# Optimization experiments

Measured on AMD Instinct MI355X. Metric: run time of the kernel, lower is better.

## Reference

```python
import jax, jax.numpy as jnp
import numpy as np

HIDDEN = 1024
NUM_HEADS = 16
HEAD_DIM = HIDDEN // NUM_HEADS
EPS = 1e-12


def _layernorm(x, g, b):
    mu = jnp.mean(x, axis=-1, keepdims=True)
    var = jnp.var(x, axis=-1, keepdims=True)
    return (x - mu) * jax.lax.rsqrt(var + EPS) * g + b


def _attention(q, k, v, mask, Wd, bd, ln_g, ln_b):
    # q: [B,T,H], k/v: [B,S,H], mask: [B,1,1,S] additive
    B, T, _ = q.shape
    S = k.shape[1]
    qh = q.reshape(B, T, NUM_HEADS, HEAD_DIM).transpose(0, 2, 1, 3)  # [B,h,T,d]
    kh = k.reshape(B, S, NUM_HEADS, HEAD_DIM).transpose(0, 2, 1, 3)
    vh = v.reshape(B, S, NUM_HEADS, HEAD_DIM).transpose(0, 2, 1, 3)
    scores = jnp.einsum('bhtd,bhsd->bhts', qh, kh) / jnp.sqrt(jnp.float32(HEAD_DIM))
    if mask is not None:
        scores = scores + mask
    probs = jax.nn.softmax(scores, axis=-1)  # dropout = identity in eval
    ctx = jnp.einsum('bhts,bhsd->bthd', probs, vh)  # [B,T,h,d]
    # torch: w = dense.weight.t().view(h, d, H); einsum('bfnd,ndh->bfh')
    w = Wd.T.reshape(NUM_HEADS, HEAD_DIM, HIDDEN)
    proj = jnp.einsum('bthd,hdH->btH', ctx, w) + bd
    # residual is the (projected) query tensor q, per source
    return _layernorm(q + proj, ln_g, ln_b)


def setup_inputs() -> dict:
    key = jax.random.key(0)
    ks = jax.random.split(key, 12)
    s = 0.02
    B, S, T = 4, 1024, 1024
    return {
        'encoder_states': jax.random.normal(ks[0], (B, S, HIDDEN), jnp.float32),
        'decoder_inputs': jax.random.normal(ks[1], (B, T, HIDDEN), jnp.float32),
        'src_attention_mask': jnp.zeros((B, 1, 1, S), jnp.float32),
        'tgt_attention_mask': jnp.zeros((B, 1, 1, T), jnp.float32),
        'Wq': jax.random.normal(ks[2], (HIDDEN, HIDDEN), jnp.float32) * s,
        'bq': jnp.zeros((HIDDEN,), jnp.float32),
        'Wk': jax.random.normal(ks[3], (HIDDEN, HIDDEN), jnp.float32) * s,
        'bk': jnp.zeros((HIDDEN,), jnp.float32),
        'Wv': jax.random.normal(ks[4], (HIDDEN, HIDDEN), jnp.float32) * s,
        'bv': jnp.zeros((HIDDEN,), jnp.float32),
        'Wd': jax.random.normal(ks[5], (HIDDEN, HIDDEN), jnp.float32) * s,
        'bd': jnp.zeros((HIDDEN,), jnp.float32),
        'ln_g': jnp.ones((HIDDEN,), jnp.float32),
        'ln_b': jnp.zeros((HIDDEN,), jnp.float32),
    }


def reference(encoder_states, decoder_inputs, src_attention_mask, tgt_attention_mask,
              Wq, bq, Wk, bk, Wv, bv, Wd, bd, ln_g, ln_b):
    # projections (torch Linear: x @ W.T + b)
    q1 = decoder_inputs @ Wq.T + bq
    k1 = decoder_inputs @ Wk.T + bk
    v1 = decoder_inputs @ Wv.T + bv
    ek = encoder_states @ Wk.T + bk
    ev = encoder_states @ Wv.T + bv
    # self-attention over decoder states
    self_out = _attention(q1, k1, v1, tgt_attention_mask, Wd, bd, ln_g, ln_b)
    # cross-attention: query = self_out directly (no extra projection, per source)
    out = _attention(self_out, ek, ev, src_attention_mask, Wd, bd, ln_g, ln_b)
    return out
```

## Files before the change

### kernel.cpp

```cpp
#include <hip/hip_runtime.h>
#include <stdint.h>


#define B_   4
#define T_   1024
#define S_   1024
#define H_   1024
#define LOG2E 1.44269504088896340736f
#define SCALE_K (0.125f * LOG2E)

typedef __attribute__((ext_vector_type(8)))  __bf16       bf16x8;
typedef __attribute__((ext_vector_type(4)))  float        f32x4;
typedef __attribute__((ext_vector_type(16))) float        f32x16;
typedef __attribute__((ext_vector_type(4)))  unsigned int uint4v;

static __device__ __forceinline__ float bf2f(unsigned int u) {
    return __builtin_bit_cast(float, u << 16);
}
static __device__ __forceinline__ unsigned short f2bf(float f) {
    unsigned int x = __builtin_bit_cast(unsigned int, f);
    return (unsigned short)((x + 0x7fffu + ((x >> 16) & 1u)) >> 16);
}
static __device__ __forceinline__ unsigned int cvt_pk_bf16(float lo, float hi) {
    unsigned int r;
    asm("v_cvt_pk_bf16_f32 %0, %1, %2" : "=v"(r) : "v"(lo), "v"(hi));
    return r;
}
static __device__ __forceinline__ void perm32swap(unsigned int& a, unsigned int& b) {
    asm("v_permlane32_swap_b32 %0, %1" : "+v"(a), "+v"(b));
}
static __device__ __forceinline__ f32x4 mfma16(bf16x8 a, bf16x8 b, f32x4 c) {
    return __builtin_amdgcn_mfma_f32_16x16x32_bf16(a, b, c, 0, 0, 0);
}
static __device__ __forceinline__ f32x16 mfma32(bf16x8 a, bf16x8 b, f32x16 c) {
    return __builtin_amdgcn_mfma_f32_32x32x16_bf16(a, b, c, 0, 0, 0);
}

typedef const __attribute__((address_space(1))) void gv_t;
typedef __attribute__((address_space(3))) void lv_t;
static __device__ __forceinline__ void g2lds16(const void* g, void* l) {
    __builtin_amdgcn_global_load_lds((gv_t*)(size_t)g, (lv_t*)(unsigned int)(size_t)l, 16, 0, 0);
}

struct CvtArgs {
    const float* src[6];
    unsigned short* dst[6];
    float scale[6];
    int n4[6];
};
__global__ __launch_bounds__(256)
void cvt_multi(CvtArgs a) {
    const int k = blockIdx.y;
    const int i = blockIdx.x * 256 + threadIdx.x;
    if (i >= a.n4[k]) return;
    const float s = a.scale[k];
    float4 v = ((const float4*)a.src[k])[i];
    uint2 o;
    o.x = (unsigned)f2bf(v.x * s) | ((unsigned)f2bf(v.y * s) << 16);
    o.y = (unsigned)f2bf(v.z * s) | ((unsigned)f2bf(v.w * s) << 16);
    ((uint2*)a.dst[k])[i] = o;
}

struct GemmJob {
    const unsigned short* A[5];
    const unsigned short* W[5];
    const float* bias[5];
    float bs[5];
    unsigned short* O[5];
    unsigned short* OT[5];
};
__global__ __launch_bounds__(256, 2)
void gemm_bf16(GemmJob job)
{
    __shared__ char smem[32768];
    char* As = smem;
    char* Bs = smem + 16384;
    const int tid = threadIdx.x;
    const int lane = tid & 63;
    const int w = tid >> 6;
    const int c = lane & 15, g = lane >> 4;
    const int wm = (w >> 1) * 64, wn = (w & 1) * 64;
    const int m0 = blockIdx.x * 128;
    const int set = blockIdx.y >> 3;
    const int n0 = (blockIdx.y & 7) * 128;
    const unsigned short* A    = job.A[set];
    const unsigned short* W    = job.W[set];
    const float* bias          = job.bias[set];
    const float bscale         = job.bs[set];
    unsigned short* O          = job.O[set];
    unsigned short* OT         = job.OT[set];

    f32x4 acc[4][4];
#pragma unroll
    for (int i = 0; i < 4; i++)
#pragma unroll
        for (int j = 0; j < 4; j++) acc[i][j] = (f32x4){0.f, 0.f, 0.f, 0.f};

    const int srow = w * 32 + (lane >> 3);
    const int swzc = ((lane & 7) ^ (lane >> 3)) * 8;
    const unsigned short* gA = A + (size_t)(m0 + srow) * 1024 + swzc;
    const unsigned short* gB = W + (size_t)(n0 + srow) * 1024 + swzc;
    char* lA = As + w * 4096;
    char* lB = Bs + w * 4096;

    for (int kk = 0; kk < 1024; kk += 64) {
#pragma unroll
        for (int q = 0; q < 4; q++) {
            g2lds16(gA + kk + q*8192, lA + q*1024);
            g2lds16(gB + kk + q*8192, lB + q*1024);
        }
        __syncthreads();
#pragma unroll
        for (int ksub = 0; ksub < 2; ksub++) {
            bf16x8 af[4], bfr[4];
#pragma unroll
            for (int t = 0; t < 4; t++) {
                const int ra = wm + t*16 + c;
                const int rb = wn + t*16 + c;
                const int so = ((ksub*4 + g) ^ (c & 7)) << 4;
                af[t]  = *(const bf16x8*)(As + ra*128 + so);
                bfr[t] = *(const bf16x8*)(Bs + rb*128 + so);
            }
#pragma unroll
            for (int i = 0; i < 4; i++)
#pragma unroll
                for (int j = 0; j < 4; j++)
                    acc[i][j] = mfma16(af[i], bfr[j], acc[i][j]);
        }
        __syncthreads();
    }

    float bvv[4];
#pragma unroll
    for (int j = 0; j < 4; j++) bvv[j] = bias[n0 + wn + j*16 + c] * bscale;

    if (OT == nullptr) {
        char* eb = As + w * 4096;
#pragma unroll
        for (int p = 0; p < 2; p++) {
#pragma unroll
            for (int ii = 0; ii < 2; ii++) {
                const int i = p*2 + ii;
#pragma unroll
                for (int j = 0; j < 4; j++)
#pragma unroll
                    for (int r = 0; r < 4; r++)
                        *(unsigned short*)(eb + (ii*16 + g*4 + r)*128 + (c + j*16)*2)
                            = f2bf(acc[i][j][r] + bvv[j]);
            }
            asm volatile("s_waitcnt lgkmcnt(0)" ::: "memory");
#pragma unroll
            for (int it = 0; it < 4; it++) {
                const int lrow = it*8 + (lane >> 3);
                uint4 vv = *(const uint4*)(eb + lrow*128 + (lane & 7)*16);
                *(uint4*)(O + (size_t)(m0 + wm + p*32 + lrow)*1024 + n0 + wn + (lane & 7)*8) = vv;
            }
            if (p == 0) asm volatile("s_waitcnt lgkmcnt(0)" ::: "memory");
        }
    } else {
        char* ebT = smem + w * 8192;
        const int n_glob = n0 + wn + lane;
        const int hh = n_glob >> 6, dd = n_glob & 63;
        const int bidx = m0 >> 10;
        unsigned short* vout0 = OT + ((size_t)((bidx*16 + hh)*64 + dd))*S_ + (m0 & 1023) + wm;
#pragma unroll
        for (int p = 0; p < 2; p++) {
#pragma unroll
            for (int ii = 0; ii < 2; ii++) {
                const int i = p*2 + ii;
#pragma unroll
                for (int j = 0; j < 4; j++) {
                    uint2 pw;
                    pw.x = (unsigned)f2bf(acc[i][j][0] + bvv[j]) |
                           ((unsigned)f2bf(acc[i][j][1] + bvv[j]) << 16);
                    pw.y = (unsigned)f2bf(acc[i][j][2] + bvv[j]) |
                           ((unsigned)f2bf(acc[i][j][3] + bvv[j]) << 16);
                    *(uint2*)(ebT + (j*16 + c)*72 + (ii*16 + g*4)*2) = pw;
                }
            }
            asm volatile("s_waitcnt lgkmcnt(0)" ::: "memory");
            unsigned short* vout = vout0 + p*32;
#pragma unroll
            for (int q = 0; q < 4; q++) {
                uint2 r0 = *(const uint2*)(ebT + lane*72 + (q*2    )*8);
                uint2 r1 = *(const uint2*)(ebT + lane*72 + (q*2 + 1)*8);
                uint4 vv; vv.x = r0.x; vv.y = r0.y; vv.z = r1.x; vv.w = r1.y;
                *(uint4*)(vout + q*8) = vv;
            }
            if (p == 0) asm volatile("s_waitcnt lgkmcnt(0)" ::: "memory");
        }
    }
}

__global__ __launch_bounds__(256, 4)
void attn_fused2(const unsigned short* __restrict__ Q,
                 const unsigned short* __restrict__ Kx,
                 const unsigned short* __restrict__ VT,
                 const float* __restrict__ mask,
                 unsigned short* __restrict__ Octx)
{
    __shared__ char smem[32768 + 4096 + 512 + 16];
    float* mb   = (float*)(smem + 32768);
    float* lbuf = (float*)(smem + 32768 + 4096);
    int* flag   = (int*)(smem + 32768 + 4096 + 512);

    const int tid = threadIdx.x;
    const int lane = tid & 63, w = tid >> 6;
    const int qc = lane & 31, hi = lane >> 5;
    const int bh = blockIdx.x, b = bh >> 4, h = bh & 15;
    const int q0 = blockIdx.y * 128 + w * 32;

    const int r0 = tid >> 3, sg = tid & 7;
    const unsigned short* gK0 = Kx + (size_t)(b*S_ + r0)*H_  + h*64 + sg*8;
    const unsigned short* gK1 = gK0 + (size_t)32*H_;
    const unsigned short* gV0 = VT + (size_t)(bh*64 + r0)*S_ + sg*8;
    const unsigned short* gV1 = gV0 + (size_t)32*S_;
    const int woff = r0*128 + ((sg*16) ^ ((r0 & 7) << 4));

    const unsigned short* qptr = Q + (size_t)(b*T_ + q0 + qc)*H_ + h*64 + hi*8;
    bf16x8 qf[4];
#pragma unroll
    for (int s = 0; s < 4; s++) qf[s] = *(const bf16x8*)(qptr + s*16);

    uint4 cK0 = *(const uint4*)gK0;
    uint4 cK1 = *(const uint4*)gK1;
    uint4 cV0 = *(const uint4*)gV0;
    uint4 cV1 = *(const uint4*)gV1;

    if (tid == 0) *flag = 0;
    __syncthreads();
    {
        float4 mv = ((const float4*)(mask + (size_t)b*S_))[tid];
        float4 ms;
        ms.x = mv.x * LOG2E; ms.y = mv.y * LOG2E; ms.z = mv.z * LOG2E; ms.w = mv.w * LOG2E;
        ((float4*)mb)[tid] = ms;
        if (mv.x != 0.f || mv.y != 0.f || mv.z != 0.f || mv.w != 0.f) atomicOr(flag, 1);
    }
    {
        char* b0 = smem;
        *(uint4*)(b0 + woff)               = cK0;
        *(uint4*)(b0 + 4096 + woff)        = cK1;
        *(uint4*)(b0 + 8192 + woff)        = cV0;
        *(uint4*)(b0 + 8192 + 4096 + woff) = cV1;
    }
    __syncthreads();
    const int msk = *flag;

    f32x16 o0 = {}, o1 = {};
    float lacc = 0.f;

    for (int t = 0; t < 16; ++t) {
        uint4 nK0, nK1, nV0, nV1;
        if (t < 15) {
            const size_t ko = (size_t)(t + 1) * 64 * H_;
            const int    vo = (t + 1) * 64;
            nK0 = *(const uint4*)(gK0 + ko);
            nK1 = *(const uint4*)(gK1 + ko);
            nV0 = *(const uint4*)(gV0 + vo);
            nV1 = *(const uint4*)(gV1 + vo);
        }
        char* Ks = smem + (t & 1) * 16384;
        char* Vs = Ks + 8192;

#pragma unroll
        for (int ts = 0; ts < 2; ++ts) {
            f32x16 st = {};
            __builtin_amdgcn_s_setprio(1);
#pragma unroll
            for (int step = 0; step < 4; ++step) {
                bf16x8 ak = *(const bf16x8*)(Ks + (ts*32 + qc)*128 +
                             ((step*32 + hi*16) ^ ((qc & 7) << 4)));
                st = mfma32(ak, qf[step], st);
            }
            __builtin_amdgcn_s_setprio(0);

            float pv[16];
            if (msk) {
#pragma unroll
                for (int rq = 0; rq < 4; ++rq) {
                    const float4 bb = *(const float4*)(mb + t*64 + ts*32 + rq*8 + hi*4);
#pragma unroll
                    for (int e = 0; e < 4; ++e)
                        pv[rq*4 + e] = __builtin_amdgcn_exp2f(st[rq*4 + e] + (&bb.x)[e]);
                }
            } else {
#pragma unroll
                for (int r = 0; r < 16; ++r) pv[r] = __builtin_amdgcn_exp2f(st[r]);
            }
#pragma unroll
            for (int r = 0; r < 16; ++r) lacc += pv[r];

#pragma unroll
            for (int half = 0; half < 2; ++half) {
                unsigned w0 = cvt_pk_bf16(pv[half*8 + 0], pv[half*8 + 1]);
                unsigned w1 = cvt_pk_bf16(pv[half*8 + 2], pv[half*8 + 3]);
                unsigned w2 = cvt_pk_bf16(pv[half*8 + 4], pv[half*8 + 5]);
                unsigned w3 = cvt_pk_bf16(pv[half*8 + 6], pv[half*8 + 7]);
                perm32swap(w0, w2);
                perm32swap(w1, w3);
                uint4v fw; fw[0] = w0; fw[1] = w1; fw[2] = w2; fw[3] = w3;
                const bf16x8 pa = __builtin_bit_cast(bf16x8, fw);
                const int scol = (ts*64 + half*32 + hi*16) ^ ((qc & 7) << 4);
                bf16x8 v0 = *(const bf16x8*)(Vs + qc*128        + scol);
                bf16x8 v1 = *(const bf16x8*)(Vs + (32 + qc)*128 + scol);
                __builtin_amdgcn_s_setprio(1);
                o0 = mfma32(pa, v0, o0);
                o1 = mfma32(pa, v1, o1);
                __builtin_amdgcn_s_setprio(0);
            }
        }

        if (t < 15) {
            char* nxt = smem + ((t + 1) & 1) * 16384;
            *(uint4*)(nxt + woff)               = nK0;
            *(uint4*)(nxt + 4096 + woff)        = nK1;
            *(uint4*)(nxt + 8192 + woff)        = nV0;
            *(uint4*)(nxt + 8192 + 4096 + woff) = nV1;
        }
        __syncthreads();
    }

    {
        unsigned la = __builtin_bit_cast(unsigned, lacc);
        unsigned lb = la;
        perm32swap(la, lb);
        const float ltot = __builtin_bit_cast(float, la) + __builtin_bit_cast(float, lb);
        const float linv = 1.f / ltot;
        if (hi == 0) lbuf[w*32 + qc] = linv;
    }
    __syncthreads();
    float4 li[4];
#pragma unroll
    for (int rq = 0; rq < 4; ++rq)
        li[rq] = *(const float4*)(lbuf + w*32 + rq*8 + hi*4);

#pragma unroll
    for (int dt = 0; dt < 2; ++dt) {
        const f32x16& oo = dt ? o1 : o0;
#pragma unroll
        for (int r = 0; r < 16; ++r) {
            const int qrow = (r & 3) + 8*(r >> 2) + 4*hi;
            const float val = oo[r] * (&li[r >> 2].x)[r & 3];
            Octx[(size_t)(b*T_ + q0 + qrow)*H_ + h*64 + dt*32 + qc] = f2bf(val);
        }
    }
}

template<int OUTMODE>
__global__ __launch_bounds__(256)
void ln_kernel(const unsigned short* __restrict__ resid,
               const unsigned short* __restrict__ proj,
               const float* __restrict__ gam,
               const float* __restrict__ bet,
               unsigned short* __restrict__ obf,
               float* __restrict__ of32)
{
    __shared__ float red[8];
    const int tid = threadIdx.x;
    const int lane = tid & 63, w = tid >> 6;
    const int i = tid * 4;
    const size_t base = (size_t)blockIdx.x * 1024 + i;
    uint2 rv = *(const uint2*)(resid + base);
    uint2 pv = *(const uint2*)(proj + base);
    float x[4];
    x[0] = bf2f(rv.x & 0xffffu) + bf2f(pv.x & 0xffffu);
    x[1] = bf2f(rv.x >> 16)     + bf2f(pv.x >> 16);
    x[2] = bf2f(rv.y & 0xffffu) + bf2f(pv.y & 0xffffu);
    x[3] = bf2f(rv.y >> 16)     + bf2f(pv.y >> 16);
    float s = x[0] + x[1] + x[2] + x[3];
    float q = x[0]*x[0] + x[1]*x[1] + x[2]*x[2] + x[3]*x[3];
#pragma unroll
    for (int off = 1; off < 64; off <<= 1) {
        s += __shfl_xor(s, off);
        q += __shfl_xor(q, off);
    }
    if (lane == 0) { red[w*2] = s; red[w*2 + 1] = q; }
    __syncthreads();
    s = red[0] + red[2] + red[4] + red[6];
    q = red[1] + red[3] + red[5] + red[7];
    const float mu   = s * (1.f/1024.f);
    const float var  = q * (1.f/1024.f) - mu*mu;
    const float rstd = rsqrtf(var + 1e-12f);
    const float4 gv = *(const float4*)(gam + i);
    const float4 bv = *(const float4*)(bet + i);
    float y[4];
#pragma unroll
    for (int j = 0; j < 4; j++)
        y[j] = (x[j] - mu) * rstd * (&gv.x)[j] + (&bv.x)[j];
    if (OUTMODE == 0) {
        uint2 oo;
        oo.x = (unsigned)f2bf(y[0]) | ((unsigned)f2bf(y[1]) << 16);
        oo.y = (unsigned)f2bf(y[2]) | ((unsigned)f2bf(y[3]) << 16);
        *(uint2*)(obf + base) = oo;
    } else {
        float4 oo; oo.x = y[0]; oo.y = y[1]; oo.z = y[2]; oo.w = y[3];
        *(float4*)(of32 + base) = oo;
    }
}

extern "C" void kernel_launch(void* const* d_in, const int* in_sizes, int n_in,
                              void* d_out, int out_size, void* d_ws, size_t ws_size,
                              hipStream_t stream)
{
    const float* enc   = (const float*)d_in[0];
    const float* dec   = (const float*)d_in[1];
    const float* smask = (const float*)d_in[2];
    const float* tmask = (const float*)d_in[3];
    const float* Wq = (const float*)d_in[4];
    const float* bq = (const float*)d_in[5];
    const float* Wk = (const float*)d_in[6];
    const float* bk = (const float*)d_in[7];
    const float* Wv = (const float*)d_in[8];
    const float* bv = (const float*)d_in[9];
    const float* Wd = (const float*)d_in[10];
    const float* bd = (const float*)d_in[11];
    const float* lng = (const float*)d_in[12];
    const float* lnb = (const float*)d_in[13];
    float* out = (float*)d_out;

    char* ws = (char*)d_ws;
    const size_t MB = 1024ull * 1024ull;
    unsigned short* dec_bf = (unsigned short*)(ws + 0*MB);
    unsigned short* enc_bf = (unsigned short*)(ws + 8*MB);
    unsigned short* Wq_bf  = (unsigned short*)(ws + 16*MB);
    unsigned short* Wk_bf  = (unsigned short*)(ws + 18*MB);
    unsigned short* Wv_bf  = (unsigned short*)(ws + 20*MB);
    unsigned short* Wd_bf  = (unsigned short*)(ws + 22*MB);
    unsigned short* q1  = (unsigned short*)(ws + 24*MB);
    unsigned short* k1  = (unsigned short*)(ws + 32*MB);
    unsigned short* vt1 = (unsigned short*)(ws + 40*MB);
    unsigned short* ek  = (unsigned short*)(ws + 48*MB);
    unsigned short* evt = (unsigned short*)(ws + 56*MB);
    unsigned short* ctx      = dec_bf;
    unsigned short* proj     = enc_bf;
    unsigned short* self_out = k1;

    CvtArgs ca;
    ca.src[0] = dec; ca.dst[0] = dec_bf; ca.scale[0] = 1.f;      ca.n4[0] = 1048576;
    ca.src[1] = enc; ca.dst[1] = enc_bf; ca.scale[1] = 1.f;      ca.n4[1] = 1048576;
    ca.src[2] = Wq;  ca.dst[2] = Wq_bf;  ca.scale[2] = 1.f;      ca.n4[2] = 262144;
    ca.src[3] = Wk;  ca.dst[3] = Wk_bf;  ca.scale[3] = SCALE_K;  ca.n4[3] = 262144;
    ca.src[4] = Wv;  ca.dst[4] = Wv_bf;  ca.scale[4] = 1.f;      ca.n4[4] = 262144;
    ca.src[5] = Wd;  ca.dst[5] = Wd_bf;  ca.scale[5] = 1.f;      ca.n4[5] = 262144;
    cvt_multi<<<dim3(4096, 6), 256, 0, stream>>>(ca);

    GemmJob j1;
    j1.A[0] = dec_bf; j1.W[0] = Wq_bf; j1.bias[0] = bq; j1.bs[0] = 1.f;     j1.O[0] = q1; j1.OT[0] = nullptr;
    j1.A[1] = dec_bf; j1.W[1] = Wk_bf; j1.bias[1] = bk; j1.bs[1] = SCALE_K; j1.O[1] = k1; j1.OT[1] = nullptr;
    j1.A[2] = dec_bf; j1.W[2] = Wv_bf; j1.bias[2] = bv; j1.bs[2] = 1.f;     j1.O[2] = nullptr; j1.OT[2] = vt1;
    j1.A[3] = enc_bf; j1.W[3] = Wk_bf; j1.bias[3] = bk; j1.bs[3] = SCALE_K; j1.O[3] = ek; j1.OT[3] = nullptr;
    j1.A[4] = enc_bf; j1.W[4] = Wv_bf; j1.bias[4] = bv; j1.bs[4] = 1.f;     j1.O[4] = nullptr; j1.OT[4] = evt;
    gemm_bf16<<<dim3(32, 40), 256, 0, stream>>>(j1);

    GemmJob jd;
    for (int i = 0; i < 5; i++) {
        jd.A[i] = ctx; jd.W[i] = Wd_bf; jd.bias[i] = bd; jd.bs[i] = 1.f;
        jd.O[i] = proj; jd.OT[i] = nullptr;
    }

    attn_fused2<<<dim3(64, 8), 256, 0, stream>>>(q1, k1, vt1, tmask, ctx);
    gemm_bf16<<<dim3(32, 8), 256, 0, stream>>>(jd);
    ln_kernel<0><<<4096, 256, 0, stream>>>(q1, proj, lng, lnb, self_out, nullptr);

    attn_fused2<<<dim3(64, 8), 256, 0, stream>>>(self_out, ek, evt, smask, ctx);
    gemm_bf16<<<dim3(32, 8), 256, 0, stream>>>(jd);
    ln_kernel<1><<<4096, 256, 0, stream>>>(self_out, proj, lng, lnb, nullptr, out);
}
```

Baseline: 165.9 us.

## Double-buffer GEMM LDS tiles and split-K the output projection

The GEMM kernel now keeps two LDS stages and issues the global-to-LDS loads for the next K tile before computing on the current one, so load latency overlaps with the MFMA work. The output-projection GEMM is split along K into two halves, which doubles its grid from 256 to 512 blocks to fill the GPU better. Each half writes its own bf16 partial result, with bias added in only one half, and the LayerNorm kernel reads and sums both partials. In exchange, LDS use per block doubles to 64KB, the GEMMs write and read one extra intermediate tensor, and the partial sums are rounded to bf16 separately.

```diff
diff --git a/kernel.cpp b/kernel.cpp
--- a/kernel.cpp
+++ b/kernel.cpp
@@ -68,13 +68,13 @@
     float bs[5];
     unsigned short* O[5];
     unsigned short* OT[5];
+    int koff[5];
+    int klen[5];
 };
 __global__ __launch_bounds__(256, 2)
 void gemm_bf16(GemmJob job)
 {
-    __shared__ char smem[32768];
-    char* As = smem;
-    char* Bs = smem + 16384;
+    __shared__ char smem[65536];
     const int tid = threadIdx.x;
     const int lane = tid & 63;
     const int w = tid >> 6;
@@ -89,6 +89,8 @@
     const float bscale         = job.bs[set];
     unsigned short* O          = job.O[set];
     unsigned short* OT         = job.OT[set];
+    const int koff             = job.koff[set];
+    const int kend             = koff + job.klen[set];
 
     f32x4 acc[4][4];
 #pragma unroll
@@ -100,16 +102,25 @@
     const int swzc = ((lane & 7) ^ (lane >> 3)) * 8;
     const unsigned short* gA = A + (size_t)(m0 + srow) * 1024 + swzc;
     const unsigned short* gB = W + (size_t)(n0 + srow) * 1024 + swzc;
-    char* lA = As + w * 4096;
-    char* lB = Bs + w * 4096;
-
-    for (int kk = 0; kk < 1024; kk += 64) {
+
+    auto stage = [&](int kk, int b) {
+        char* dA = smem + b*32768 +         w*4096;
+        char* dB = smem + b*32768 + 16384 + w*4096;
 #pragma unroll
         for (int q = 0; q < 4; q++) {
-            g2lds16(gA + kk + q*8192, lA + q*1024);
-            g2lds16(gB + kk + q*8192, lB + q*1024);
-        }
-        __syncthreads();
+            g2lds16(gA + kk + q*8192, dA + q*1024);
+            g2lds16(gB + kk + q*8192, dB + q*1024);
+        }
+    };
+
+    stage(koff, 0);
+    __syncthreads();
+
+    int bi = 0;
+    for (int kk = koff; kk < kend; kk += 64, bi ^= 1) {
+        if (kk + 64 < kend) stage(kk + 64, bi ^ 1);
+        const char* As = smem + bi*32768;
+        const char* Bs = As + 16384;
 #pragma unroll
         for (int ksub = 0; ksub < 2; ksub++) {
             bf16x8 af[4], bfr[4];
@@ -135,7 +146,7 @@
     for (int j = 0; j < 4; j++) bvv[j] = bias[n0 + wn + j*16 + c] * bscale;
 
     if (OT == nullptr) {
-        char* eb = As + w * 4096;
+        char* eb = smem + w * 4096;
 #pragma unroll
         for (int p = 0; p < 2; p++) {
 #pragma unroll
@@ -349,7 +360,8 @@
 template<int OUTMODE>
 __global__ __launch_bounds__(256)
 void ln_kernel(const unsigned short* __restrict__ resid,
-               const unsigned short* __restrict__ proj,
+               const unsigned short* __restrict__ projA,
+               const unsigned short* __restrict__ projB,
                const float* __restrict__ gam,
                const float* __restrict__ bet,
                unsigned short* __restrict__ obf,
@@ -361,12 +373,13 @@
     const int i = tid * 4;
     const size_t base = (size_t)blockIdx.x * 1024 + i;
     uint2 rv = *(const uint2*)(resid + base);
-    uint2 pv = *(const uint2*)(proj + base);
+    uint2 pv = *(const uint2*)(projA + base);
+    uint2 qv = *(const uint2*)(projB + base);
     float x[4];
-    x[0] = bf2f(rv.x & 0xffffu) + bf2f(pv.x & 0xffffu);
-    x[1] = bf2f(rv.x >> 16)     + bf2f(pv.x >> 16);
-    x[2] = bf2f(rv.y & 0xffffu) + bf2f(pv.y & 0xffffu);
-    x[3] = bf2f(rv.y >> 16)     + bf2f(pv.y >> 16);
+    x[0] = bf2f(rv.x & 0xffffu) + bf2f(pv.x & 0xffffu) + bf2f(qv.x & 0xffffu);
+    x[1] = bf2f(rv.x >> 16)     + bf2f(pv.x >> 16)     + bf2f(qv.x >> 16);
+    x[2] = bf2f(rv.y & 0xffffu) + bf2f(pv.y & 0xffffu) + bf2f(qv.y & 0xffffu);
+    x[3] = bf2f(rv.y >> 16)     + bf2f(pv.y >> 16)     + bf2f(qv.y >> 16);
     float s = x[0] + x[1] + x[2] + x[3];
     float q = x[0]*x[0] + x[1]*x[1] + x[2]*x[2] + x[3]*x[3];
 #pragma unroll
@@ -433,6 +446,7 @@
     unsigned short* evt = (unsigned short*)(ws + 56*MB);
     unsigned short* ctx      = dec_bf;
     unsigned short* proj     = enc_bf;
+    unsigned short* projb    = vt1;
     unsigned short* self_out = k1;
 
     CvtArgs ca;
@@ -450,19 +464,21 @@
     j1.A[2] = dec_bf; j1.W[2] = Wv_bf; j1.bias[2] = bv; j1.bs[2] = 1.f;     j1.O[2] = nullptr; j1.OT[2] = vt1;
     j1.A[3] = enc_bf; j1.W[3] = Wk_bf; j1.bias[3] = bk; j1.bs[3] = SCALE_K; j1.O[3] = ek; j1.OT[3] = nullptr;
     j1.A[4] = enc_bf; j1.W[4] = Wv_bf; j1.bias[4] = bv; j1.bs[4] = 1.f;     j1.O[4] = nullptr; j1.OT[4] = evt;
+    for (int i = 0; i < 5; i++) { j1.koff[i] = 0; j1.klen[i] = 1024; }
     gemm_bf16<<<dim3(32, 40), 256, 0, stream>>>(j1);
 
     GemmJob jd;
     for (int i = 0; i < 5; i++) {
         jd.A[i] = ctx; jd.W[i] = Wd_bf; jd.bias[i] = bd; jd.bs[i] = 1.f;
-        jd.O[i] = proj; jd.OT[i] = nullptr;
-    }
+        jd.O[i] = proj; jd.OT[i] = nullptr; jd.koff[i] = 0; jd.klen[i] = 512;
+    }
+    jd.bs[1] = 0.f; jd.O[1] = projb; jd.koff[1] = 512;
 
     attn_fused2<<<dim3(64, 8), 256, 0, stream>>>(q1, k1, vt1, tmask, ctx);
-    gemm_bf16<<<dim3(32, 8), 256, 0, stream>>>(jd);
-    ln_kernel<0><<<4096, 256, 0, stream>>>(q1, proj, lng, lnb, self_out, nullptr);
+    gemm_bf16<<<dim3(32, 16), 256, 0, stream>>>(jd);
+    ln_kernel<0><<<4096, 256, 0, stream>>>(q1, proj, projb, lng, lnb, self_out, nullptr);
 
     attn_fused2<<<dim3(64, 8), 256, 0, stream>>>(self_out, ek, evt, smask, ctx);
-    gemm_bf16<<<dim3(32, 8), 256, 0, stream>>>(jd);
-    ln_kernel<1><<<4096, 256, 0, stream>>>(self_out, proj, lng, lnb, nullptr, out);
-}
+    gemm_bf16<<<dim3(32, 16), 256, 0, stream>>>(jd);
+    ln_kernel<1><<<4096, 256, 0, stream>>>(self_out, proj, projb, lng, lnb, nullptr, out);
+}
```

New measurement: 155.3 us. 6.4% less time.
